# Performance work log

Measured on AMD Instinct MI355X. Metric: run time of the kernel, lower is better.

## Reference

```python
import jax, jax.numpy as jnp
import numpy as np
from jax import lax

Bsz, C, Hd, Wd = 4, 96, 64, 64
DI, N, R = 192, 16, 6   # d_inner = 2*C, d_state, dt_rank = ceil(C/16)
L = Hd * Wd
KDIRS = 4


def dwconv(x, w, dilation=1):
    # x: (B,C,H,W), w: (C,1,k,k) depthwise, 'same' padding for odd k
    k = w.shape[-1]
    p = dilation * (k - 1) // 2
    return lax.conv_general_dilated(
        x, w, window_strides=(1, 1), padding=[(p, p), (p, p)],
        rhs_dilation=(dilation, dilation),
        dimension_numbers=('NCHW', 'OIHW', 'NCHW'),
        feature_group_count=x.shape[1])


def setup_inputs() -> dict:
    key = jax.random.key(0)
    ks = jax.random.split(key, 24)
    def nrm(i, shape, s=0.02):
        return jax.random.normal(ks[i], shape, jnp.float32) * s
    return {
        'x': jax.random.normal(ks[0], (Bsz, C, Hd, Wd), jnp.float32),
        'w_lk': nrm(1, (C, 1, 13, 13)),
        'w_k5': nrm(2, (C, 1, 5, 5)),
        'w_k7': nrm(3, (C, 1, 7, 7)),
        'w_k9': nrm(4, (C, 1, 9, 9)),
        'w_k3d4': nrm(5, (C, 1, 3, 3)),
        'w_k3d5': nrm(6, (C, 1, 3, 3)),
        'w_k3d6': nrm(7, (C, 1, 3, 3)),
        'bn_scale': jax.random.uniform(ks[8], (7, C), jnp.float32, 0.5, 1.5),
        'bn_shift': nrm(9, (7, C), 0.01),
        'in_proj_w': nrm(10, (2 * DI, C)),
        'conv2d_w': nrm(11, (DI, 1, 3, 3)),
        'conv2d_b': nrm(12, (DI,), 0.01),
        'x_proj_w': nrm(13, (KDIRS, R + 2 * N, DI)),
        'dt_projs_w': nrm(14, (KDIRS, DI, R), 0.1),
        'dt_projs_b': jax.random.uniform(ks[15], (KDIRS, DI), jnp.float32, -4.0, -2.0),
        'A_logs': jnp.log(jnp.tile(jnp.arange(1, N + 1, dtype=jnp.float32), (KDIRS, DI, 1))),
        'Ds': jnp.ones((KDIRS, DI), jnp.float32),
        'ln_gamma': jnp.ones((DI,), jnp.float32),
        'ln_beta': jnp.zeros((DI,), jnp.float32),
        'out_proj_w': nrm(16, (C, DI)),
    }


def reference(x, w_lk, w_k5, w_k7, w_k9, w_k3d4, w_k3d5, w_k3d6, bn_scale, bn_shift,
              in_proj_w, conv2d_w, conv2d_b, x_proj_w, dt_projs_w, dt_projs_b,
              A_logs, Ds, ln_gamma, ln_beta, out_proj_w):
    # --- DilatedReparamBlock: LK depthwise conv + parallel dilated DW branches, BN folded to per-channel scale/shift (eval) ---
    branches = [(w_lk, 1), (w_k5, 1), (w_k7, 2), (w_k9, 3), (w_k3d4, 4), (w_k3d5, 5), (w_k3d6, 6)]
    y = jnp.zeros_like(x)
    for i, (w, d) in enumerate(branches):
        y = y + dwconv(x, w, d) * bn_scale[i][None, :, None, None] + bn_shift[i][None, :, None, None]
    # --- SS2D_v3: 4-direction 2D selective scan (VMamba-style) ---
    xhwc = y.transpose(0, 2, 3, 1)                       # B,H,W,C
    xz = xhwc @ in_proj_w.T                              # B,H,W,2*DI
    xpart, z = jnp.split(xz, 2, axis=-1)
    xc = xpart.transpose(0, 3, 1, 2)                     # B,DI,H,W
    xc = jax.nn.silu(dwconv(xc, conv2d_w, 1) + conv2d_b[None, :, None, None])
    x_hw = xc.reshape(Bsz, DI, L)                        # row-major scan
    x_wh = xc.transpose(0, 1, 3, 2).reshape(Bsz, DI, L)  # col-major scan
    xs = jnp.stack([x_hw, x_wh, x_hw[:, :, ::-1], x_wh[:, :, ::-1]], axis=1)  # B,4,DI,L
    x_dbl = jnp.einsum('bkdl,kcd->bkcl', xs, x_proj_w)
    dts, Bs, Cs = jnp.split(x_dbl, [R, R + N], axis=2)
    dts = jnp.einsum('bkrl,kdr->bkdl', dts, dt_projs_w) + dt_projs_b[None, :, :, None]
    delta = jax.nn.softplus(dts)                          # B,4,DI,L
    A = -jnp.exp(A_logs)                                  # 4,DI,N

    def step(h, inp):
        d_t, b_t, c_t, u_t = inp                          # (B,4,DI),(B,4,N),(B,4,N),(B,4,DI)
        h = jnp.exp(d_t[..., None] * A) * h + (d_t * u_t)[..., None] * b_t[:, :, None, :]
        return h, jnp.einsum('bkdn,bkn->bkd', h, c_t)

    h0 = jnp.zeros((Bsz, KDIRS, DI, N), x.dtype)
    seq = (delta.transpose(3, 0, 1, 2), Bs.transpose(3, 0, 1, 2),
           Cs.transpose(3, 0, 1, 2), xs.transpose(3, 0, 1, 2))
    _, ys = lax.scan(step, h0, seq)                       # L,B,4,DI
    ys = ys.transpose(1, 2, 3, 0) + Ds[None, :, :, None] * xs  # B,4,DI,L
    y0 = ys[:, 0]
    y1 = ys[:, 1].reshape(Bsz, DI, Wd, Hd).transpose(0, 1, 3, 2).reshape(Bsz, DI, L)
    y2 = ys[:, 2, :, ::-1]
    y3 = ys[:, 3, :, ::-1].reshape(Bsz, DI, Wd, Hd).transpose(0, 1, 3, 2).reshape(Bsz, DI, L)
    yo = (y0 + y1 + y2 + y3).transpose(0, 2, 1).reshape(Bsz, Hd, Wd, DI)
    mu = yo.mean(-1, keepdims=True)
    var = yo.var(-1, keepdims=True)
    yo = (yo - mu) / jnp.sqrt(var + 1e-5) * ln_gamma + ln_beta   # LayerNorm
    yo = yo * jax.nn.silu(z)
    out = (yo @ out_proj_w.T).transpose(0, 3, 1, 2)       # B,C,H,W
    return jnp.clip(out, 0.0, 6.0)                        # ReLU6
```

## Files before the change

### kernel.cpp

```cpp
#include <hip/hip_runtime.h>
#include <hip/hip_bf16.h>

typedef __hip_bfloat16 bf16;

__device__ __align__(16) float g_wcat[96*352];
__device__ float g_shift[96];
__device__ __align__(16) float g_win[96*384];
__device__ __align__(16) float g_wx[4*192*40];
__device__ __align__(16) float g_wo[192*96];
__device__ __align__(16) float g_xq[4*96*88*88];
__device__ __align__(16) float g_cw[192*9];
__device__ float g_cb[192];
__device__ float g_dtw[4*192*6];
__device__ float g_dtb[4*192];
__device__ float g_alog[4*192*16];
__device__ float g_dsp[4*192];
__device__ float g_gam[192];
__device__ float g_bet[192];
__device__ __align__(16) float g_y1[4*96*4096];
__device__ __align__(16) float g_zs[4*4096*192];
__device__ __align__(16) float g_xp[4*4096*192];
__device__ __align__(16) float g_xc[4*4096*192];
__device__ __align__(16) float g_xd[16*4096*40];
__device__ float g_cs[16*128*192];
__device__ __align__(16) float g_ch[16*128*192*16];
__device__ __align__(16) float g_hin[16*128*192*16];
__device__ __align__(16) float g_ys[16*4096*192];

__device__ __forceinline__ bool is_bf16(const void* gam){
    return ((const unsigned short*)gam)[0] == 0x3F80u;
}
__device__ __forceinline__ float ldin(const void* p, int i, bool b){
    return b ? __bfloat162float(((const bf16*)p)[i]) : ((const float*)p)[i];
}

__device__ __forceinline__ int usp(int k, int l){
    int j = (k & 2) ? (4095 - l) : l;
    if (k & 1) j = ((j & 63) << 6) | (j >> 6);
    return j;
}

__global__ __launch_bounds__(256) void kc_convert(
    const void* x, const void* cw, const void* cb, const void* dtw, const void* dtb,
    const void* alog, const void* dsp, const void* gam, const void* bet)
{
    bool bf = is_bf16(gam);
    int i = blockIdx.x * 256 + threadIdx.x;
    if (i < 2973696){
        int bc = i / 7744, rc = i % 7744;
        int rr = rc / 88, cc = rc % 88;
        int gh = rr - 12, gw = cc - 12;
        float v = 0.f;
        if (gh >= 0 && gh < 64 && gw >= 0 && gw < 64)
            v = ldin(x, (bc << 12) + (gh << 6) + gw, bf);
        g_xq[i] = v;
        return;
    }
    i -= 2973696;
    if (i < 1728){ g_cw[i] = ldin(cw, i, bf); return; }
    i -= 1728;
    if (i < 192){ g_cb[i] = ldin(cb, i, bf); return; }
    i -= 192;
    if (i < 4608){ g_dtw[i] = ldin(dtw, i, bf); return; }
    i -= 4608;
    if (i < 768){ g_dtb[i] = ldin(dtb, i, bf); return; }
    i -= 768;
    if (i < 12288){ g_alog[i] = ldin(alog, i, bf); return; }
    i -= 12288;
    if (i < 768){ g_dsp[i] = ldin(dsp, i, bf); return; }
    i -= 768;
    if (i < 192){ g_gam[i] = ldin(gam, i, bf); return; }
    i -= 192;
    if (i < 192){ g_bet[i] = ldin(bet, i, bf); return; }
}

__global__ __launch_bounds__(256) void k0_prep(
    const void* wlk, const void* w5, const void* w7, const void* w9,
    const void* w34, const void* w35, const void* w36,
    const void* bscale, const void* bshift,
    const void* winp, const void* xpw, const void* outw, const void* gam)
{
    bool bf = is_bf16(gam);
    int i = blockIdx.x * 256 + threadIdx.x;
    if (i < 33792){
        int c = i / 352, t = i % 352;
        float v = 0.f;
        if (t < 351){
            const void* wp; int br, ks, ti;
            if      (t < 169){ wp=wlk; br=0; ks=13; ti=t; }
            else if (t < 194){ wp=w5;  br=1; ks=5;  ti=t-169; }
            else if (t < 243){ wp=w7;  br=2; ks=7;  ti=t-194; }
            else if (t < 324){ wp=w9;  br=3; ks=9;  ti=t-243; }
            else if (t < 333){ wp=w34; br=4; ks=3;  ti=t-324; }
            else if (t < 342){ wp=w35; br=5; ks=3;  ti=t-333; }
            else             { wp=w36; br=6; ks=3;  ti=t-342; }
            v = ldin(wp, c*ks*ks + ti, bf) * ldin(bscale, br*96 + c, bf);
        }
        g_wcat[i] = v;
        return;
    }
    i -= 33792;
    if (i < 96){
        float s = 0.f;
        for (int q = 0; q < 7; ++q) s += ldin(bshift, q*96 + i, bf);
        g_shift[i] = s;
        return;
    }
    i -= 96;
    if (i < 36864){ int c = i/384, j = i%384; g_win[i] = ldin(winp, j*96 + c, bf); return; }
    i -= 36864;
    if (i < 30720){
        int k = i/7680; int rem = i%7680; int dd = rem/40; int c = rem%40;
        g_wx[i] = (c < 38) ? ldin(xpw, (k*38 + c)*192 + dd, bf) : 0.f;
        return;
    }
    i -= 30720;
    if (i < 18432){ int dd = i/96, c = i%96; g_wo[i] = ldin(outw, c*192 + dd, bf); return; }
}

__global__ __launch_bounds__(256) void k1_dwconv()
{
    int bid = blockIdx.x;
    int ht = bid & 3;
    int bc = bid >> 2; int c = bc % 96; int b = bc / 96;
    int r  = threadIdx.x >> 4;
    int w0 = (threadIdx.x & 15) << 2;
    int h = (ht << 4) + r;

    const float* xq = g_xq + (long)bc * 7744;
    const float* wc = g_wcat + c*352;

    float acc[4];
    float sh = g_shift[c];
#pragma unroll
    for (int p = 0; p < 4; ++p) acc[p] = sh;

    int t = 0;
#define BRANCH(K, D, ST, NF4) { const int off = (K-1)/2; \
    _Pragma("unroll") \
    for (int kh = 0; kh < K; ++kh){ \
        const float* row = xq + (h + 12 + D*(kh - off))*88 + (w0 + 12 + (ST)); \
        float rx[(NF4)*4]; \
        _Pragma("unroll") \
        for (int q = 0; q < (NF4); ++q) *(float4*)&rx[q*4] = *(const float4*)&row[q*4]; \
        _Pragma("unroll") \
        for (int kw = 0; kw < K; ++kw){ \
            float wv = wc[t + kh*K + kw]; \
            const int dl = D*(kw - off) - (ST); \
            _Pragma("unroll") \
            for (int p = 0; p < 4; ++p) acc[p] = fmaf(rx[dl + p], wv, acc[p]); \
        } \
    } t += K*K; }
    BRANCH(13,1, -8,5)
    BRANCH( 5,1, -4,3)
    BRANCH( 7,2, -8,5)
    BRANCH( 9,3,-12,7)
    BRANCH( 3,4, -4,3)
    BRANCH( 3,5, -8,5)
    BRANCH( 3,6, -8,5)
#undef BRANCH

    float* yo = g_y1 + ((long)bc << 12) + (h << 6) + w0;
    *(float4*)yo = make_float4(acc[0], acc[1], acc[2], acc[3]);
}

__global__ __launch_bounds__(384) void k2_inproj()
{
    __shared__ __align__(16) float ysh[96][64];
    __shared__ __align__(16) float wsh[96][96];
    int blk = blockIdx.x;
    int jt = blk & 3; int pt = blk >> 2;
    int b = pt >> 6; int l0 = (pt & 63) << 6;
    int tid = threadIdx.x;

    for (int i = tid; i < 96*64; i += 384){
        int c = i >> 6, pl = i & 63;
        ysh[c][pl] = g_y1[((b*96 + c) << 12) + l0 + pl];
    }
    for (int i = tid; i < 96*96; i += 384){
        int c = i / 96, jj = i % 96;
        wsh[c][jj] = g_win[c*384 + jt*96 + jj];
    }
    __syncthreads();

    int jgrp = tid % 24, pgrp = tid / 24;
    int jj0 = jgrp * 4, pl0 = pgrp * 4;
    float acc[4][4];
#pragma unroll
    for (int p = 0; p < 4; ++p)
#pragma unroll
        for (int q = 0; q < 4; ++q) acc[p][q] = 0.f;

    for (int c = 0; c < 96; ++c){
        float4 a = *(const float4*)&ysh[c][pl0];
        float4 wv = *(const float4*)&wsh[c][jj0];
        float av[4] = {a.x, a.y, a.z, a.w};
        float wvv[4] = {wv.x, wv.y, wv.z, wv.w};
#pragma unroll
        for (int p = 0; p < 4; ++p)
#pragma unroll
            for (int q = 0; q < 4; ++q) acc[p][q] = fmaf(av[p], wvv[q], acc[p][q]);
    }

    bool isx = (jt < 2);
    float* dst = isx ? g_xp : g_zs;
    int jb = (isx ? jt : (jt - 2)) * 96 + jj0;
#pragma unroll
    for (int p = 0; p < 4; ++p){
        int l = l0 + pl0 + p;
        float4 o;
        if (isx){
            o = make_float4(acc[p][0], acc[p][1], acc[p][2], acc[p][3]);
        } else {
            float v0 = acc[p][0], v1 = acc[p][1], v2 = acc[p][2], v3 = acc[p][3];
            o = make_float4(v0 / (1.f + __expf(-v0)), v1 / (1.f + __expf(-v1)),
                            v2 / (1.f + __expf(-v2)), v3 / (1.f + __expf(-v3)));
        }
        *(float4*)&dst[(b*4096 + l)*192 + jb] = o;
    }
}

__global__ __launch_bounds__(192) void k3_conv3()
{
    int l = blockIdx.x & 4095; int b = blockIdx.x >> 12;
    int d = threadIdx.x;
    int h = l >> 6, w = l & 63;
    const float* xp = g_xp + b*4096*192;
    float acc = g_cb[d];
#pragma unroll
    for (int kh = 0; kh < 3; ++kh){
        int hh = h + kh - 1;
        if (hh < 0 || hh >= 64) continue;
#pragma unroll
        for (int kw = 0; kw < 3; ++kw){
            int wp = w + kw - 1;
            if (wp < 0 || wp >= 64) continue;
            acc = fmaf(xp[((hh << 6) + wp)*192 + d], g_cw[d*9 + kh*3 + kw], acc);
        }
    }
    float v = acc / (1.f + __expf(-acc));
    g_xc[(b*4096 + l)*192 + d] = v;
}

__global__ __launch_bounds__(256) void k4_xdbl()
{
    __shared__ __align__(16) float xs[48][68];
    __shared__ __align__(16) float wsh[48][160];
    int blk = blockIdx.x;
    int b = blk >> 6;
    int j0 = (blk & 63) << 6;
    int tid = threadIdx.x;
    int pg = tid >> 4;
    int cg = tid & 15;
    int kdir = cg >> 2;
    int c0 = (cg & 3) * 10;

    float acc[4][10];
#pragma unroll
    for (int p = 0; p < 4; ++p)
#pragma unroll
        for (int c = 0; c < 10; ++c) acc[p][c] = 0.f;

    const float* xc = g_xc + b*4096*192;

    for (int d0 = 0; d0 < 192; d0 += 48){
        for (int i = tid; i < 768; i += 256){
            int d4 = i % 12, p = i / 12;
            const float4 v = *(const float4*)&xc[(j0 + p)*192 + d0 + d4*4];
            xs[d4*4+0][p] = v.x; xs[d4*4+1][p] = v.y;
            xs[d4*4+2][p] = v.z; xs[d4*4+3][p] = v.w;
        }
        for (int i = tid; i < 7680; i += 256){
            int c = i % 160, d = i / 160;
            int k = c / 40, cc = c % 40;
            wsh[d][c] = g_wx[k*7680 + (d0 + d)*40 + cc];
        }
        __syncthreads();
#pragma unroll 4
        for (int kk = 0; kk < 48; ++kk){
            float4 xv = *(const float4*)&xs[kk][pg*4];
            const float* wr = &wsh[kk][kdir*40 + c0];
            float xa[4] = {xv.x, xv.y, xv.z, xv.w};
#pragma unroll
            for (int c = 0; c < 10; ++c){
                float wv = wr[c];
#pragma unroll
                for (int p = 0; p < 4; ++p) acc[p][c] = fmaf(xa[p], wv, acc[p][c]);
            }
        }
        __syncthreads();
    }

#pragma unroll
    for (int p = 0; p < 4; ++p){
        int j = j0 + pg*4 + p;
        int jt = ((j & 63) << 6) | (j >> 6);
        int l;
        if      (kdir == 0) l = j;
        else if (kdir == 1) l = jt;
        else if (kdir == 2) l = 4095 - j;
        else                l = 4095 - jt;
        float* out = g_xd + ((long)(((b*4 + kdir) << 12) + l))*40 + c0;
#pragma unroll
        for (int c = 0; c < 10; c += 2)
            *(float2*)&out[c] = make_float2(acc[p][c], acc[p][c+1]);
    }
}

template<int WRITE_Y>
__global__ __launch_bounds__(192) void kscan()
{
    int blk = blockIdx.x;
    int ch = blk & 127; int bk = blk >> 7;
    int k = bk & 3; int b = bk >> 2;
    int d = threadIdx.x;

    float wdt[6];
#pragma unroll
    for (int r = 0; r < 6; ++r) wdt[r] = g_dtw[(k*192 + d)*6 + r];
    float bias = g_dtb[k*192 + d];
    float f[16];
#pragma unroll
    for (int n = 0; n < 16; ++n){
        float mA = __expf(g_alog[(k*192 + d)*16 + n]);
        f[n] = mA - (float)(n + 1);
    }

    const float* xd = g_xd + ((long)(bk << 12) + (ch << 5))*40;
    const float* xc = g_xc + b*4096*192;
    int ci = (bk*128 + ch)*192 + d;
    int lbase = ch << 5;

    float h[16];
    if (WRITE_Y){
        const float* hin = g_hin + (long)ci*16;
#pragma unroll
        for (int n = 0; n < 16; ++n) h[n] = hin[n];
    } else {
#pragma unroll
        for (int n = 0; n < 16; ++n) h[n] = 0.f;
    }
    float Dsv = WRITE_Y ? g_dsp[k*192 + d] : 0.f;
    float S = 0.f;

    constexpr int NQ = WRITE_Y ? 10 : 6;
    float bufA[NQ*4], bufB[NQ*4];

#pragma unroll
    for (int q = 0; q < NQ; ++q) *(float4*)&bufA[q*4] = *(const float4*)&xd[q*4];
    float uA = xc[usp(k, lbase)*192 + d];

#define STEP(BUF, UV, RR) { \
    float dtv = bias; \
    _Pragma("unroll") \
    for (int q = 0; q < 6; ++q) dtv = fmaf(BUF[q], wdt[q], dtv); \
    float t = __expf(dtv); \
    float delta = (dtv > 15.f) ? dtv : __logf(1.f + t); \
    float e1 = __builtin_amdgcn_rcpf(1.f + t); \
    float du = delta * (UV); \
    S += delta; \
    float e2 = e1*e1, e4 = e2*e2, e8 = e4*e4; \
    float pw[16]; \
    pw[0]=e1;      pw[1]=e2;      pw[2]=e2*e1;   pw[3]=e4; \
    pw[4]=e4*e1;   pw[5]=e4*e2;   pw[6]=pw[5]*e1; pw[7]=e8; \
    pw[8]=e8*e1;   pw[9]=e8*e2;   pw[10]=pw[9]*e1; pw[11]=e8*e4; \
    pw[12]=pw[11]*e1; pw[13]=pw[11]*e2; pw[14]=pw[13]*e1; pw[15]=e8*e8; \
    float md = -delta; \
    float y0=0.f, y1=0.f, y2=0.f, y3=0.f; \
    _Pragma("unroll") \
    for (int n = 0; n < 16; ++n){ \
        float wv = fmaf(md * f[n], pw[n], pw[n]); \
        h[n] = fmaf(wv, h[n], du * BUF[6 + n]); \
        if (WRITE_Y){ \
            if ((n & 3) == 0) y0 = fmaf(h[n], BUF[22 + n], y0); \
            if ((n & 3) == 1) y1 = fmaf(h[n], BUF[22 + n], y1); \
            if ((n & 3) == 2) y2 = fmaf(h[n], BUF[22 + n], y2); \
            if ((n & 3) == 3) y3 = fmaf(h[n], BUF[22 + n], y3); \
        } \
    } \
    if (WRITE_Y) \
        g_ys[((long)(bk << 12) + lbase + (RR))*192 + d] = (y0 + y1) + (y2 + y3) + Dsv * (UV); }

    for (int r = 0; r < 32; r += 2){
        const float* rp1 = xd + (r + 1)*40;
#pragma unroll
        for (int q = 0; q < NQ; ++q) *(float4*)&bufB[q*4] = *(const float4*)&rp1[q*4];
        float uB = xc[usp(k, lbase + r + 1)*192 + d];

        STEP(bufA, uA, r)

        if (r + 2 < 32){
            const float* rp2 = xd + (r + 2)*40;
#pragma unroll
            for (int q = 0; q < NQ; ++q) *(float4*)&bufA[q*4] = *(const float4*)&rp2[q*4];
            uA = xc[usp(k, lbase + r + 2)*192 + d];
        }

        STEP(bufB, uB, r + 1)
    }
#undef STEP

    if (!WRITE_Y){
        g_cs[ci] = S;
        float* chp = g_ch + (long)ci*16;
#pragma unroll
        for (int n = 0; n < 16; ++n) chp[n] = h[n];
    }
}

__global__ __launch_bounds__(256) void kB_carry()
{
    int t = blockIdx.x * 256 + threadIdx.x;
    int n = t & 15;
    int d = (t >> 4) % 192;
    int bk = t / 3072;
    int k = bk & 3;
    float A = -__expf(g_alog[(k*192 + d)*16 + n]);
    float h = 0.f;
#pragma unroll 8
    for (int c = 0; c < 128; ++c){
        int ci = (bk*128 + c)*192 + d;
        g_hin[(long)ci*16 + n] = h;
        float S = g_cs[ci];
        h = __expf(A * S) * h + g_ch[(long)ci*16 + n];
    }
}

__global__ __launch_bounds__(256) void k6_out(void* outp, const void* gamraw)
{
    __shared__ __align__(16) float gs_t[192*68];
    __shared__ __align__(16) float wsh[48][96];
    bool bf = is_bf16(gamraw);
    int blk = blockIdx.x;
    int b = blk >> 6;
    int l0 = (blk & 63) << 6;
    int tid = threadIdx.x;

    {
        int p = tid >> 2;
        int q = tid & 3;
        int d0 = q * 48;
        int l = l0 + p;
        int l1 = ((l & 63) << 6) | (l >> 6);
        int base = (b * 4) << 12;
        const float* r0 = g_ys + (long)(base + l)*192 + d0;
        const float* r1 = g_ys + (long)(base + 4096 + l1)*192 + d0;
        const float* r2 = g_ys + (long)(base + 8192 + (4095 - l))*192 + d0;
        const float* r3 = g_ys + (long)(base + 12288 + (4095 - l1))*192 + d0;

        float v[48];
#pragma unroll
        for (int i = 0; i < 12; ++i){
            float4 a = *(const float4*)&r0[i*4];
            float4 c = *(const float4*)&r1[i*4];
            float4 e = *(const float4*)&r2[i*4];
            float4 g = *(const float4*)&r3[i*4];
            v[i*4+0] = a.x + c.x + e.x + g.x;
            v[i*4+1] = a.y + c.y + e.y + g.y;
            v[i*4+2] = a.z + c.z + e.z + g.z;
            v[i*4+3] = a.w + c.w + e.w + g.w;
        }
        float s = 0.f, ss = 0.f;
#pragma unroll
        for (int i = 0; i < 48; ++i){ s += v[i]; ss += v[i]*v[i]; }
        s  += __shfl_xor(s, 1, 64);  ss += __shfl_xor(ss, 1, 64);
        s  += __shfl_xor(s, 2, 64);  ss += __shfl_xor(ss, 2, 64);
        float mu = s * (1.f/192.f);
        float var = ss * (1.f/192.f) - mu*mu;
        float rs = rsqrtf(var + 1e-5f);

        const float* zp = g_zs + (long)(b*4096 + l)*192 + d0;
#pragma unroll
        for (int i = 0; i < 48; i += 4){
            float4 z4 = *(const float4*)&zp[i];
            float4 gm = *(const float4*)&g_gam[d0 + i];
            float4 bt = *(const float4*)&g_bet[d0 + i];
            gs_t[(d0+i+0)*68 + p] = ((v[i+0]-mu)*rs*gm.x + bt.x) * z4.x;
            gs_t[(d0+i+1)*68 + p] = ((v[i+1]-mu)*rs*gm.y + bt.y) * z4.y;
            gs_t[(d0+i+2)*68 + p] = ((v[i+2]-mu)*rs*gm.z + bt.z) * z4.z;
            gs_t[(d0+i+3)*68 + p] = ((v[i+3]-mu)*rs*gm.w + bt.w) * z4.w;
        }
    }
    __syncthreads();

    int pg = tid >> 4;
    int og = tid & 15;
    int px0 = pg * 4, o0 = og * 6;
    float acc[4][6];
#pragma unroll
    for (int p = 0; p < 4; ++p)
#pragma unroll
        for (int o = 0; o < 6; ++o) acc[p][o] = 0.f;

    for (int kc = 0; kc < 4; ++kc){
        for (int i = tid; i < 1152; i += 256){
            int row = i / 24, col = (i % 24) * 4;
            *(float4*)&wsh[row][col] = *(const float4*)&g_wo[(kc*48 + row)*96 + col];
        }
        __syncthreads();
#pragma unroll 4
        for (int kk = 0; kk < 48; ++kk){
            float4 gv = *(const float4*)&gs_t[(kc*48 + kk)*68 + px0];
            float2 w0 = *(const float2*)&wsh[kk][o0];
            float2 w1 = *(const float2*)&wsh[kk][o0+2];
            float2 w2 = *(const float2*)&wsh[kk][o0+4];
            float ga[4] = {gv.x, gv.y, gv.z, gv.w};
            float wa[6] = {w0.x, w0.y, w1.x, w1.y, w2.x, w2.y};
#pragma unroll
            for (int o = 0; o < 6; ++o)
#pragma unroll
                for (int p = 0; p < 4; ++p) acc[p][o] = fmaf(ga[p], wa[o], acc[p][o]);
        }
        __syncthreads();
    }

#pragma unroll
    for (int o = 0; o < 6; ++o){
        long oi = ((long)(b*96 + o0 + o) << 12) + l0 + px0;
        float c0 = fminf(fmaxf(acc[0][o], 0.f), 6.f);
        float c1 = fminf(fmaxf(acc[1][o], 0.f), 6.f);
        float c2 = fminf(fmaxf(acc[2][o], 0.f), 6.f);
        float c3 = fminf(fmaxf(acc[3][o], 0.f), 6.f);
        if (bf){
            union { bf16 b4[4]; ushort4 u; } t;
            t.b4[0] = __float2bfloat16(c0); t.b4[1] = __float2bfloat16(c1);
            t.b4[2] = __float2bfloat16(c2); t.b4[3] = __float2bfloat16(c3);
            *(ushort4*)&((bf16*)outp)[oi] = t.u;
        } else {
            *(float4*)&((float*)outp)[oi] = make_float4(c0, c1, c2, c3);
        }
    }
}

extern "C" void kernel_launch(void* const* d_in, const int* in_sizes, int n_in,
                              void* d_out, int out_size, void* d_ws, size_t ws_size,
                              hipStream_t stream)
{
    const void* x     = d_in[0];
    const void* wlk   = d_in[1];
    const void* w5    = d_in[2];
    const void* w7    = d_in[3];
    const void* w9    = d_in[4];
    const void* w34   = d_in[5];
    const void* w35   = d_in[6];
    const void* w36   = d_in[7];
    const void* bsc   = d_in[8];
    const void* bsh   = d_in[9];
    const void* winp  = d_in[10];
    const void* cw    = d_in[11];
    const void* cb    = d_in[12];
    const void* xpw   = d_in[13];
    const void* dtw   = d_in[14];
    const void* dtb   = d_in[15];
    const void* alog  = d_in[16];
    const void* dsp   = d_in[17];
    const void* gam   = d_in[18];
    const void* bet   = d_in[19];
    const void* outw  = d_in[20];

    kc_convert<<<11697, 256, 0, stream>>>(x, cw, cb, dtw, dtb, alog, dsp, gam, bet);
    k0_prep<<<469, 256, 0, stream>>>(wlk, w5, w7, w9, w34, w35, w36, bsc, bsh, winp, xpw, outw, gam);
    k1_dwconv<<<4*96*4, 256, 0, stream>>>();
    k2_inproj<<<1024, 384, 0, stream>>>();
    k3_conv3<<<4*4096, 192, 0, stream>>>();
    k4_xdbl<<<256, 256, 0, stream>>>();
    kscan<0><<<2048, 192, 0, stream>>>();
    kB_carry<<<192, 256, 0, stream>>>();
    kscan<1><<<2048, 192, 0, stream>>>();
    k6_out<<<256, 256, 0, stream>>>(d_out, gam);
}
```

Baseline: 388.9 us.

## Store conv activations and scan outputs in bf16, merge prep kernels

The intermediate buffers g_xc (post-conv SiLU activations) and g_ys (per-direction scan outputs) become bf16 instead of fp32, and the consumer kernels (x_dbl projection, both scan passes, output/LayerNorm) unpack them with 128-bit loads. This halves the memory traffic for these large intermediates, especially the 4-direction gather in the output kernel. Separately, the two setup kernels for input conversion and weight prep are fused into one launch. The cost is reduced precision in the scan input u and in the summed outputs ahead of LayerNorm, which could affect accuracy tolerance.

```diff
diff --git a/kernel.cpp b/kernel.cpp
--- a/kernel.cpp
+++ b/kernel.cpp
@@ -20,18 +20,25 @@
 __device__ __align__(16) float g_y1[4*96*4096];
 __device__ __align__(16) float g_zs[4*4096*192];
 __device__ __align__(16) float g_xp[4*4096*192];
-__device__ __align__(16) float g_xc[4*4096*192];
+__device__ __align__(16) bf16  g_xc[4*4096*192];
 __device__ __align__(16) float g_xd[16*4096*40];
 __device__ float g_cs[16*128*192];
 __device__ __align__(16) float g_ch[16*128*192*16];
 __device__ __align__(16) float g_hin[16*128*192*16];
-__device__ __align__(16) float g_ys[16*4096*192];
+__device__ __align__(16) bf16  g_ys[16*4096*192];
 
 __device__ __forceinline__ bool is_bf16(const void* gam){
     return ((const unsigned short*)gam)[0] == 0x3F80u;
 }
 __device__ __forceinline__ float ldin(const void* p, int i, bool b){
     return b ? __bfloat162float(((const bf16*)p)[i]) : ((const float*)p)[i];
+}
+__device__ __forceinline__ float b2f(unsigned u){ return __uint_as_float(u << 16); }
+__device__ __forceinline__ void u4_to_f8(uint4 v, float* o){
+    o[0]=b2f(v.x&0xffffu); o[1]=b2f(v.x>>16);
+    o[2]=b2f(v.y&0xffffu); o[3]=b2f(v.y>>16);
+    o[4]=b2f(v.z&0xffffu); o[5]=b2f(v.z>>16);
+    o[6]=b2f(v.w&0xffffu); o[7]=b2f(v.w>>16);
 }
 
 __device__ __forceinline__ int usp(int k, int l){
@@ -40,9 +47,13 @@
     return j;
 }
 
-__global__ __launch_bounds__(256) void kc_convert(
+__global__ __launch_bounds__(256) void kc_all(
     const void* x, const void* cw, const void* cb, const void* dtw, const void* dtb,
-    const void* alog, const void* dsp, const void* gam, const void* bet)
+    const void* alog, const void* dsp, const void* gam, const void* bet,
+    const void* wlk, const void* w5, const void* w7, const void* w9,
+    const void* w34, const void* w35, const void* w36,
+    const void* bscale, const void* bshift,
+    const void* winp, const void* xpw, const void* outw)
 {
     bool bf = is_bf16(gam);
     int i = blockIdx.x * 256 + threadIdx.x;
@@ -72,16 +83,7 @@
     if (i < 192){ g_gam[i] = ldin(gam, i, bf); return; }
     i -= 192;
     if (i < 192){ g_bet[i] = ldin(bet, i, bf); return; }
-}
-
-__global__ __launch_bounds__(256) void k0_prep(
-    const void* wlk, const void* w5, const void* w7, const void* w9,
-    const void* w34, const void* w35, const void* w36,
-    const void* bscale, const void* bshift,
-    const void* winp, const void* xpw, const void* outw, const void* gam)
-{
-    bool bf = is_bf16(gam);
-    int i = blockIdx.x * 256 + threadIdx.x;
+    i -= 192;
     if (i < 33792){
         int c = i / 352, t = i % 352;
         float v = 0.f;
@@ -239,7 +241,7 @@
         }
     }
     float v = acc / (1.f + __expf(-acc));
-    g_xc[(b*4096 + l)*192 + d] = v;
+    g_xc[(b*4096 + l)*192 + d] = __float2bfloat16(v);
 }
 
 __global__ __launch_bounds__(256) void k4_xdbl()
@@ -261,14 +263,16 @@
 #pragma unroll
         for (int c = 0; c < 10; ++c) acc[p][c] = 0.f;
 
-    const float* xc = g_xc + b*4096*192;
+    const unsigned short* xcb = (const unsigned short*)g_xc + (long)b*4096*192;
 
     for (int d0 = 0; d0 < 192; d0 += 48){
-        for (int i = tid; i < 768; i += 256){
-            int d4 = i % 12, p = i / 12;
-            const float4 v = *(const float4*)&xc[(j0 + p)*192 + d0 + d4*4];
-            xs[d4*4+0][p] = v.x; xs[d4*4+1][p] = v.y;
-            xs[d4*4+2][p] = v.z; xs[d4*4+3][p] = v.w;
+        for (int i = tid; i < 384; i += 256){
+            int d8 = i % 6, p = i / 6;
+            uint4 v = *(const uint4*)(xcb + (long)(j0 + p)*192 + d0 + d8*8);
+            float f8[8];
+            u4_to_f8(v, f8);
+#pragma unroll
+            for (int j = 0; j < 8; ++j) xs[d8*8 + j][p] = f8[j];
         }
         for (int i = tid; i < 7680; i += 256){
             int c = i % 160, d = i / 160;
@@ -327,7 +331,7 @@
     }
 
     const float* xd = g_xd + ((long)(bk << 12) + (ch << 5))*40;
-    const float* xc = g_xc + b*4096*192;
+    const bf16* xc = g_xc + (long)b*4096*192;
     int ci = (bk*128 + ch)*192 + d;
     int lbase = ch << 5;
 
@@ -348,7 +352,7 @@
 
 #pragma unroll
     for (int q = 0; q < NQ; ++q) *(float4*)&bufA[q*4] = *(const float4*)&xd[q*4];
-    float uA = xc[usp(k, lbase)*192 + d];
+    float uA = __bfloat162float(xc[usp(k, lbase)*192 + d]);
 
 #define STEP(BUF, UV, RR) { \
     float dtv = bias; \
@@ -379,13 +383,14 @@
         } \
     } \
     if (WRITE_Y) \
-        g_ys[((long)(bk << 12) + lbase + (RR))*192 + d] = (y0 + y1) + (y2 + y3) + Dsv * (UV); }
+        g_ys[((long)(bk << 12) + lbase + (RR))*192 + d] = \
+            __float2bfloat16((y0 + y1) + (y2 + y3) + Dsv * (UV)); }
 
     for (int r = 0; r < 32; r += 2){
         const float* rp1 = xd + (r + 1)*40;
 #pragma unroll
         for (int q = 0; q < NQ; ++q) *(float4*)&bufB[q*4] = *(const float4*)&rp1[q*4];
-        float uB = xc[usp(k, lbase + r + 1)*192 + d];
+        float uB = __bfloat162float(xc[usp(k, lbase + r + 1)*192 + d]);
 
         STEP(bufA, uA, r)
 
@@ -393,7 +398,7 @@
             const float* rp2 = xd + (r + 2)*40;
 #pragma unroll
             for (int q = 0; q < NQ; ++q) *(float4*)&bufA[q*4] = *(const float4*)&rp2[q*4];
-            uA = xc[usp(k, lbase + r + 2)*192 + d];
+            uA = __bfloat162float(xc[usp(k, lbase + r + 2)*192 + d]);
         }
 
         STEP(bufB, uB, r + 1)
@@ -443,22 +448,22 @@
         int l = l0 + p;
         int l1 = ((l & 63) << 6) | (l >> 6);
         int base = (b * 4) << 12;
-        const float* r0 = g_ys + (long)(base + l)*192 + d0;
-        const float* r1 = g_ys + (long)(base + 4096 + l1)*192 + d0;
-        const float* r2 = g_ys + (long)(base + 8192 + (4095 - l))*192 + d0;
-        const float* r3 = g_ys + (long)(base + 12288 + (4095 - l1))*192 + d0;
+        const unsigned short* ysu = (const unsigned short*)g_ys;
+        const unsigned short* r0 = ysu + (long)(base + l)*192 + d0;
+        const unsigned short* r1 = ysu + (long)(base + 4096 + l1)*192 + d0;
+        const unsigned short* r2 = ysu + (long)(base + 8192 + (4095 - l))*192 + d0;
+        const unsigned short* r3 = ysu + (long)(base + 12288 + (4095 - l1))*192 + d0;
 
         float v[48];
 #pragma unroll
-        for (int i = 0; i < 12; ++i){
-            float4 a = *(const float4*)&r0[i*4];
-            float4 c = *(const float4*)&r1[i*4];
-            float4 e = *(const float4*)&r2[i*4];
-            float4 g = *(const float4*)&r3[i*4];
-            v[i*4+0] = a.x + c.x + e.x + g.x;
-            v[i*4+1] = a.y + c.y + e.y + g.y;
-            v[i*4+2] = a.z + c.z + e.z + g.z;
-            v[i*4+3] = a.w + c.w + e.w + g.w;
+        for (int i = 0; i < 6; ++i){
+            float ta[8], tc[8], te[8], tg[8];
+            u4_to_f8(*(const uint4*)(r0 + i*8), ta);
+            u4_to_f8(*(const uint4*)(r1 + i*8), tc);
+            u4_to_f8(*(const uint4*)(r2 + i*8), te);
+            u4_to_f8(*(const uint4*)(r3 + i*8), tg);
+#pragma unroll
+            for (int j = 0; j < 8; ++j) v[i*8 + j] = (ta[j] + tc[j]) + (te[j] + tg[j]);
         }
         float s = 0.f, ss = 0.f;
 #pragma unroll
@@ -558,8 +563,9 @@
     const void* bet   = d_in[19];
     const void* outw  = d_in[20];
 
-    kc_convert<<<11697, 256, 0, stream>>>(x, cw, cb, dtw, dtb, alog, dsp, gam, bet);
-    k0_prep<<<469, 256, 0, stream>>>(wlk, w5, w7, w9, w34, w35, w36, bsc, bsh, winp, xpw, outw, gam);
+    kc_all<<<12167, 256, 0, stream>>>(x, cw, cb, dtw, dtb, alog, dsp, gam, bet,
+                                      wlk, w5, w7, w9, w34, w35, w36, bsc, bsh,
+                                      winp, xpw, outw);
     k1_dwconv<<<4*96*4, 256, 0, stream>>>();
     k2_inproj<<<1024, 384, 0, stream>>>();
     k3_conv3<<<4*4096, 192, 0, stream>>>();
```

Result: faster. 379.2 us (-2.5%).
